# Kernel tuning notes

Hardware: AMD Instinct MI355X
Metric: run time of the kernel (lower is better)

Reference implementation:

```python
import jax, jax.numpy as jnp
import numpy as np

D_MODEL = 1024
NUM_HEADS = 16


def setup_inputs() -> dict:
    key = jax.random.key(0)
    ks = jax.random.split(key, 5)
    B, S, D = 2, 2048, D_MODEL
    scale = 1.0 / np.sqrt(D)
    return {
        "x": jax.random.normal(ks[0], (B, S, D), dtype=jnp.float32),
        "q_proj_weight": jax.random.normal(ks[1], (D, D), dtype=jnp.float32) * scale,
        "k_proj_weight": jax.random.normal(ks[2], (D, D), dtype=jnp.float32) * scale,
        "v_proj_weight": jax.random.normal(ks[3], (D, D), dtype=jnp.float32) * scale,
        "o_proj_weight": jax.random.normal(ks[4], (D, D), dtype=jnp.float32) * scale,
    }


def _attn(x, qw, kw, vw, ow, num_heads):
    B, S, D = x.shape
    d_k = D // num_heads
    q = x @ qw.T  # [B,S,D]
    k = x @ kw.T
    v = x @ vw.T
    # split heads: [B, H, S, d_k]
    q = q.reshape(B, S, num_heads, d_k).transpose(0, 2, 1, 3)
    k = k.reshape(B, S, num_heads, d_k).transpose(0, 2, 1, 3)
    v = v.reshape(B, S, num_heads, d_k).transpose(0, 2, 1, 3)
    scores = jnp.einsum('bhqd,bhkd->bhqk', q, k) / jnp.sqrt(jnp.asarray(d_k, x.dtype))
    causal = jnp.tril(jnp.ones((S, S), dtype=bool))  # [S,S]
    scores = jnp.where(causal[None, None], scores, jnp.asarray(-jnp.inf, x.dtype))
    attn = jax.nn.softmax(scores, axis=-1)
    out = jnp.einsum('bhqk,bhkd->bhqd', attn, v)  # [B,H,S,d_k]
    out = out.transpose(0, 2, 1, 3).reshape(B, S, D)
    return out @ ow.T


def reference(x, q_proj_weight, k_proj_weight, v_proj_weight, o_proj_weight):
    return _attn(x, q_proj_weight, k_proj_weight, v_proj_weight, o_proj_weight, NUM_HEADS)
```

## Files before the change

### kernel.cpp

```cpp
#include <hip/hip_runtime.h>

typedef __attribute__((ext_vector_type(8))) short short8;
typedef __attribute__((ext_vector_type(4))) float f32x4;

#define MFMA(a,b,c) __builtin_amdgcn_mfma_f32_16x16x32_bf16((a),(b),(c),0,0,0)

#define B_  2
#define S_  2048
#define D_  1024
#define H_  16
#define DK  64
#define KDIM 1024

typedef unsigned int u32;
typedef __attribute__((address_space(1))) const u32 gu32;
typedef __attribute__((address_space(3))) u32 lu32;

__device__ __forceinline__ void gll16(const unsigned short* g, unsigned short* l){
  __builtin_amdgcn_global_load_lds((gu32*)g, (lu32*)l, 16, 0, 0);
}

__device__ __forceinline__ unsigned short f2bf(float f){
  unsigned int u = __float_as_uint(f);
  u += 0x7fffu + ((u >> 16) & 1u);
  return (unsigned short)(u >> 16);
}

__device__ __forceinline__ u32 pkbf(float lo, float hi){
  u32 a = __float_as_uint(lo) + 0x8000u;
  u32 b = __float_as_uint(hi) + 0x8000u;
  return __builtin_amdgcn_perm(b, a, 0x07060302u);
}

__global__ void cvt_all(const float* __restrict__ x,  const float* __restrict__ qw,
                        const float* __restrict__ kw, const float* __restrict__ vw,
                        const float* __restrict__ ow,
                        unsigned short* __restrict__ xb,  unsigned short* __restrict__ wqb,
                        unsigned short* __restrict__ wkb, unsigned short* __restrict__ wvb,
                        unsigned short* __restrict__ wob,
                        int n4x, int n4w){
  int i = blockIdx.x * 256 + threadIdx.x;
  const float* src; unsigned short* dst; int n4;
  switch (blockIdx.y) {
    case 0:  src = x;  dst = xb;  n4 = n4x; break;
    case 1:  src = qw; dst = wqb; n4 = n4w; break;
    case 2:  src = kw; dst = wkb; n4 = n4w; break;
    case 3:  src = vw; dst = wvb; n4 = n4w; break;
    default: src = ow; dst = wob; n4 = n4w; break;
  }
  if (i >= n4) return;
  float4 f = reinterpret_cast<const float4*>(src)[i];
  ushort4 u;
  u.x = f2bf(f.x); u.y = f2bf(f.y); u.z = f2bf(f.z); u.w = f2bf(f.w);
  reinterpret_cast<ushort4*>(dst)[i] = u;
}

struct FragsQKV { short8 a0[4], a1[4], b0[3][2], b1[3][2]; };

__global__ __launch_bounds__(256, 2) void gemm_qkv(
    const unsigned short* __restrict__ X,
    const unsigned short* __restrict__ Wq,
    const unsigned short* __restrict__ Wk,
    const unsigned short* __restrict__ Wv,
    unsigned short* __restrict__ Qo,
    unsigned short* __restrict__ Ko,
    unsigned short* __restrict__ Vo)
{
  const int n0 = blockIdx.x * 64;
  const int m0 = blockIdx.y * 128;

  __shared__ unsigned short As[2][128 * 64];
  __shared__ unsigned short Bs[2][3][64 * 64];

  const int tid  = threadIdx.x;
  const int wid  = tid >> 6, lane = tid & 63;
  const int wm   = (wid >> 1) * 64, wn = (wid & 1) * 32;
  const int lr   = lane & 15, c = lane >> 4;
  const int sw   = lr & 7;
  const int pc0  = (c ^ sw) * 8;
  const int pc1  = ((c ^ 4) ^ sw) * 8;

  const int srow = lane >> 3;
  const int scol = ((lane & 7) ^ srow) * 8;
  const unsigned short* gA  = X  + (size_t)(m0 + wid * 32 + srow) * KDIM + scol;
  const unsigned short* gBq = Wq + (size_t)(n0 + wid * 16 + srow) * KDIM + scol;
  const unsigned short* gBk = Wk + (size_t)(n0 + wid * 16 + srow) * KDIM + scol;
  const unsigned short* gBv = Wv + (size_t)(n0 + wid * 16 + srow) * KDIM + scol;

  auto stage = [&](int buf, int k0) {
    unsigned short* la  = &As[buf][(wid * 32) * 64];
    unsigned short* lbq = &Bs[buf][0][(wid * 16) * 64];
    unsigned short* lbk = &Bs[buf][1][(wid * 16) * 64];
    unsigned short* lbv = &Bs[buf][2][(wid * 16) * 64];
#pragma unroll
    for (int i = 0; i < 4; i++) gll16(gA + (size_t)(i * 8) * KDIM + k0, la + i * 512);
#pragma unroll
    for (int i = 0; i < 2; i++) gll16(gBq + (size_t)(i * 8) * KDIM + k0, lbq + i * 512);
#pragma unroll
    for (int i = 0; i < 2; i++) gll16(gBk + (size_t)(i * 8) * KDIM + k0, lbk + i * 512);
#pragma unroll
    for (int i = 0; i < 2; i++) gll16(gBv + (size_t)(i * 8) * KDIM + k0, lbv + i * 512);
  };

  auto ldfr = [&](int buf, FragsQKV& f) {
    const unsigned short* AS = As[buf];
#pragma unroll
    for (int i = 0; i < 4; i++) {
      f.a0[i] = *(const short8*)&AS[(wm + i * 16 + lr) * 64 + pc0];
      f.a1[i] = *(const short8*)&AS[(wm + i * 16 + lr) * 64 + pc1];
    }
#pragma unroll
    for (int z = 0; z < 3; z++) {
      const unsigned short* BS = Bs[buf][z];
#pragma unroll
      for (int j = 0; j < 2; j++) {
        f.b0[z][j] = *(const short8*)&BS[(wn + j * 16 + lr) * 64 + pc0];
        f.b1[z][j] = *(const short8*)&BS[(wn + j * 16 + lr) * 64 + pc1];
      }
    }
  };

  f32x4 acc[3][4][2];
  const f32x4 z4 = {0.f, 0.f, 0.f, 0.f};
#pragma unroll
  for (int z = 0; z < 3; z++)
    for (int i = 0; i < 4; i++)
      for (int j = 0; j < 2; j++) acc[z][i][j] = z4;

  auto mfmas = [&](const FragsQKV& f) {
#pragma unroll
    for (int z = 0; z < 3; z++) {
      if (z == 2) {
#pragma unroll
        for (int i = 0; i < 4; i++)
#pragma unroll
          for (int j = 0; j < 2; j++) {
            acc[z][i][j] = MFMA(f.b0[z][j], f.a0[i], acc[z][i][j]);
            acc[z][i][j] = MFMA(f.b1[z][j], f.a1[i], acc[z][i][j]);
          }
      } else {
#pragma unroll
        for (int i = 0; i < 4; i++)
#pragma unroll
          for (int j = 0; j < 2; j++) {
            acc[z][i][j] = MFMA(f.a0[i], f.b0[z][j], acc[z][i][j]);
            acc[z][i][j] = MFMA(f.a1[i], f.b1[z][j], acc[z][i][j]);
          }
      }
    }
  };

  stage(0, 0);
  stage(1, 64);

  FragsQKV f;
  const int NT = KDIM / 64;
  for (int t = 0; t < NT - 2; ++t) {
    const int buf = t & 1;
    asm volatile("s_waitcnt vmcnt(10)" ::: "memory");
    __builtin_amdgcn_s_barrier();
    asm volatile("" ::: "memory");
    ldfr(buf, f);
    asm volatile("s_waitcnt lgkmcnt(0)" ::: "memory");
    __builtin_amdgcn_sched_barrier(0);
    __builtin_amdgcn_s_barrier();
    asm volatile("" ::: "memory");
    stage(buf, (t + 2) * 64);
    __builtin_amdgcn_sched_barrier(0);
    mfmas(f);
  }
  asm volatile("s_waitcnt vmcnt(10)" ::: "memory");
  __builtin_amdgcn_s_barrier();
  asm volatile("" ::: "memory");
  ldfr((NT - 2) & 1, f);
  mfmas(f);
  asm volatile("s_waitcnt vmcnt(0)" ::: "memory");
  __builtin_amdgcn_s_barrier();
  asm volatile("" ::: "memory");
  ldfr((NT - 1) & 1, f);
  mfmas(f);

  const int rbase = (lane >> 4) * 4;
  for (int i = 0; i < 4; i++)
    for (int j = 0; j < 2; j++)
      for (int r = 0; r < 4; r++) {
        int m = m0 + wm + i * 16 + rbase + r;
        int n = n0 + wn + j * 16 + lr;
        int bb = m >> 11, s = m & 2047, h = n >> 6, d = n & 63;
        float vq = acc[0][i][j][r] * 0.18033688f;
        Qo[(((bb * H_ + h) * S_) + s) * DK + d] = f2bf(vq);
        Ko[(((bb * H_ + h) * S_) + s) * DK + d] = f2bf(acc[1][i][j][r]);
      }
  for (int i = 0; i < 4; i++)
    for (int j = 0; j < 2; j++)
      for (int r = 0; r < 4; r++) {
        int dfull = n0 + wn + j * 16 + rbase + r;
        int sfull = m0 + wm + i * 16 + lr;
        int h = dfull >> 6, d = dfull & 63;
        int bb = sfull >> 11, s = sfull & 2047;
        Vo[(((bb * H_ + h) * DK) + d) * S_ + s] = f2bf(acc[2][i][j][r]);
      }
}

__global__ __launch_bounds__(512, 4) void attn(
    const unsigned short* __restrict__ Q,
    const unsigned short* __restrict__ K,
    const unsigned short* __restrict__ V,
    unsigned short* __restrict__ O)
{
  const int h = blockIdx.y, b = blockIdx.z;
  const int qt = b ? (15 - blockIdx.x) : blockIdx.x;

  const unsigned short* __restrict__ Qh = Q + (size_t)((b * H_ + h) * S_) * DK;
  const unsigned short* __restrict__ Kh = K + (size_t)((b * H_ + h) * S_) * DK;
  const unsigned short* __restrict__ Vh = V + (size_t)((b * H_ + h) * DK) * S_;

  __shared__ unsigned short Ks0[64 * 64];
  __shared__ unsigned short Ks1[64 * 64];
  __shared__ unsigned short Vs0[64 * 64];
  __shared__ unsigned short Vs1[64 * 64];
  __shared__ unsigned short Ps[8][16][72];

  const int tid = threadIdx.x, wid = tid >> 6, lane = tid & 63;
  const int lr = lane & 15;
  const int row4 = (lane >> 4) * 4;
  const int q0 = qt * 128;
  const int qcol = q0 + wid * 16 + lr;
  const int qwmin = q0 + wid * 16;
  const int qwmax = qwmin + 15;
  const int lk = (lane >> 4) * 8;

  const int pc0 = (((lane >> 4) + lr) & 7) * 8;
  const int pc1 = (((lane >> 4) + 4 + lr) & 7) * 8;

  const int sr8 = lane >> 3;
  const int sc8 = lane & 7;
  const int sg  = (sc8 - sr8) & 7;
  const int stRow = wid * 8 + sr8;
  const unsigned short* gK = Kh + (size_t)stRow * DK + sg * 8;
  const unsigned short* gV = Vh + (size_t)stRow * S_ + sg * 8;
  unsigned short* lK0 = &Ks0[wid * 8 * 64];
  unsigned short* lK1 = &Ks1[wid * 8 * 64];
  unsigned short* lV0 = &Vs0[wid * 8 * 64];
  unsigned short* lV1 = &Vs1[wid * 8 * 64];

  const short ONE = (short)0x3F80;
  const short8 ones = {ONE, ONE, ONE, ONE, ONE, ONE, ONE, ONE};

  short8 qf[2];
  qf[0] = *(const short8*)&Qh[(q0 + wid * 16 + lr) * DK + lk];
  qf[1] = *(const short8*)&Qh[(q0 + wid * 16 + lr) * DK + 32 + lk];

  const f32x4 z4 = {0.f, 0.f, 0.f, 0.f};
  f32x4 o[4];
  for (int i = 0; i < 4; i++) o[i] = z4;
  f32x4 rs = z4;

  auto tile = [&](int k0, const unsigned short* KS, const unsigned short* VS){
    if (k0 > qwmax) return;
    f32x4 sc[4];
    __builtin_amdgcn_s_setprio(1);
    for (int nt = 0; nt < 4; nt++) {
      short8 kb0 = *(const short8*)&KS[(nt * 16 + lr) * 64 + pc0];
      short8 kb1 = *(const short8*)&KS[(nt * 16 + lr) * 64 + pc1];
      f32x4 s = MFMA(kb0, qf[0], z4);
      sc[nt] = MFMA(kb1, qf[1], s);
    }
    __builtin_amdgcn_s_setprio(0);
    if (k0 + 63 > qwmin) {
      for (int nt = 0; nt < 4; nt++) {
        int kg = k0 + nt * 16 + row4;
        for (int r = 0; r < 4; r++)
          if (kg + r > qcol) sc[nt][r] = -INFINITY;
      }
    }
    for (int nt = 0; nt < 4; nt++) {
      float p0 = __builtin_amdgcn_exp2f(sc[nt][0]);
      float p1 = __builtin_amdgcn_exp2f(sc[nt][1]);
      float p2 = __builtin_amdgcn_exp2f(sc[nt][2]);
      float p3 = __builtin_amdgcn_exp2f(sc[nt][3]);
      uint2 pk;
      pk.x = pkbf(p0, p1);
      pk.y = pkbf(p2, p3);
      *(uint2*)&Ps[wid][lr][nt * 16 + row4] = pk;
    }
    short8 pf0 = *(const short8*)&Ps[wid][lr][lk];
    short8 pf1 = *(const short8*)&Ps[wid][lr][32 + lk];
    __builtin_amdgcn_s_setprio(1);
    rs = MFMA(ones, pf0, rs);
    rs = MFMA(ones, pf1, rs);
    for (int dt = 0; dt < 4; dt++) {
      short8 vb0 = *(const short8*)&VS[(dt * 16 + lr) * 64 + pc0];
      short8 vb1 = *(const short8*)&VS[(dt * 16 + lr) * 64 + pc1];
      o[dt] = MFMA(vb0, pf0, o[dt]);
      o[dt] = MFMA(vb1, pf1, o[dt]);
    }
    __builtin_amdgcn_s_setprio(0);
  };

  const int kt_end = 2 * qt + 2;

  gll16(gK, lK0);
  gll16(gV, lV0);

  for (int kt = 0; kt < kt_end; kt += 2) {
    const int k0 = kt * 64;
    __syncthreads();
    {
      gll16(gK + (size_t)(k0 + 64) * DK, lK1);
      gll16(gV + (k0 + 64),              lV1);
    }
    tile(k0, Ks0, Vs0);
    __syncthreads();
    if (kt + 2 < kt_end) {
      gll16(gK + (size_t)(k0 + 128) * DK, lK0);
      gll16(gV + (k0 + 128),              lV0);
    }
    tile(k0 + 64, Ks1, Vs1);
  }

  const float inv = 1.0f / rs[0];

  const int srow = q0 + wid * 16 + lr;
  for (int dt = 0; dt < 4; dt++) {
    uint2 pk;
    pk.x = pkbf(o[dt][0] * inv, o[dt][1] * inv);
    pk.y = pkbf(o[dt][2] * inv, o[dt][3] * inv);
    *(uint2*)&O[(size_t)(b * S_ + srow) * D_ + h * DK + dt * 16 + row4] = pk;
  }
}

struct Frags { short8 a0[4], a1[4], b0[2], b1[2]; };

__global__ __launch_bounds__(256) void gemm_oproj(
    const unsigned short* __restrict__ A,
    const unsigned short* __restrict__ W,
    float* __restrict__ out)
{
  const int n0 = blockIdx.x * 64;
  const int m0 = blockIdx.y * 128;

  __shared__ unsigned short As[2][128 * 64];
  __shared__ unsigned short Bs[2][64 * 64];

  const int tid  = threadIdx.x;
  const int wid  = tid >> 6, lane = tid & 63;
  const int wm   = (wid >> 1) * 64, wn = (wid & 1) * 32;
  const int lr   = lane & 15, c = lane >> 4;
  const int sw   = lr & 7;
  const int pc0  = (c ^ sw) * 8;
  const int pc1  = ((c ^ 4) ^ sw) * 8;

  const int srow = lane >> 3;
  const int scol = ((lane & 7) ^ srow) * 8;
  const unsigned short* gA = A + (size_t)(m0 + wid * 32 + srow) * KDIM + scol;
  const unsigned short* gB = W + (size_t)(n0 + wid * 16 + srow) * KDIM + scol;

  auto stage = [&](int buf, int k0) {
    unsigned short* la = &As[buf][(wid * 32) * 64];
    unsigned short* lb = &Bs[buf][(wid * 16) * 64];
#pragma unroll
    for (int i = 0; i < 4; i++) gll16(gA + (size_t)(i * 8) * KDIM + k0, la + i * 512);
#pragma unroll
    for (int i = 0; i < 2; i++) gll16(gB + (size_t)(i * 8) * KDIM + k0, lb + i * 512);
  };

  auto ldfr = [&](int buf, Frags& f) {
    const unsigned short* AS = As[buf];
    const unsigned short* BS = Bs[buf];
#pragma unroll
    for (int i = 0; i < 4; i++) {
      f.a0[i] = *(const short8*)&AS[(wm + i * 16 + lr) * 64 + pc0];
      f.a1[i] = *(const short8*)&AS[(wm + i * 16 + lr) * 64 + pc1];
    }
#pragma unroll
    for (int j = 0; j < 2; j++) {
      f.b0[j] = *(const short8*)&BS[(wn + j * 16 + lr) * 64 + pc0];
      f.b1[j] = *(const short8*)&BS[(wn + j * 16 + lr) * 64 + pc1];
    }
  };

  f32x4 acc[4][2];
  const f32x4 z4 = {0.f, 0.f, 0.f, 0.f};
  for (int i = 0; i < 4; i++)
    for (int j = 0; j < 2; j++) acc[i][j] = z4;

  auto mfmas = [&](const Frags& f) {
#pragma unroll
    for (int i = 0; i < 4; i++)
#pragma unroll
      for (int j = 0; j < 2; j++) {
        acc[i][j] = MFMA(f.a0[i], f.b0[j], acc[i][j]);
        acc[i][j] = MFMA(f.a1[i], f.b1[j], acc[i][j]);
      }
  };

  stage(0, 0);
  stage(1, 64);

  Frags f;
  const int NT = KDIM / 64;
  for (int t = 0; t < NT - 2; ++t) {
    const int buf = t & 1;
    asm volatile("s_waitcnt vmcnt(6)" ::: "memory");
    __builtin_amdgcn_s_barrier();
    asm volatile("" ::: "memory");
    ldfr(buf, f);
    asm volatile("s_waitcnt lgkmcnt(0)" ::: "memory");
    __builtin_amdgcn_sched_barrier(0);
    __builtin_amdgcn_s_barrier();
    asm volatile("" ::: "memory");
    stage(buf, (t + 2) * 64);
    __builtin_amdgcn_sched_barrier(0);
    mfmas(f);
  }
  asm volatile("s_waitcnt vmcnt(6)" ::: "memory");
  __builtin_amdgcn_s_barrier();
  asm volatile("" ::: "memory");
  ldfr((NT - 2) & 1, f);
  mfmas(f);
  asm volatile("s_waitcnt vmcnt(0)" ::: "memory");
  __builtin_amdgcn_s_barrier();
  asm volatile("" ::: "memory");
  ldfr((NT - 1) & 1, f);
  mfmas(f);

  const int rbase = (lane >> 4) * 4;
  for (int i = 0; i < 4; i++)
    for (int j = 0; j < 2; j++)
      for (int r = 0; r < 4; r++) {
        int m = m0 + wm + i * 16 + rbase + r;
        int n = n0 + wn + j * 16 + lr;
        out[(size_t)m * D_ + n] = acc[i][j][r];
      }
}

extern "C" void kernel_launch(void* const* d_in, const int* in_sizes, int n_in,
                              void* d_out, int out_size, void* d_ws, size_t ws_size,
                              hipStream_t stream) {
  const float* x  = (const float*)d_in[0];
  const float* qw = (const float*)d_in[1];
  const float* kw = (const float*)d_in[2];
  const float* vw = (const float*)d_in[3];
  const float* ow = (const float*)d_in[4];
  float* out = (float*)d_out;

  char* ws = (char*)d_ws;
  size_t off = 0;
  auto alloc = [&](size_t bytes) -> void* {
    void* p = ws + off;
    off += (bytes + 255) & ~(size_t)255;
    return p;
  };
  const size_t XN = (size_t)B_ * S_ * D_;
  const size_t WN = (size_t)D_ * D_;
  unsigned short* xb  = (unsigned short*)alloc(XN * 2);
  unsigned short* wqb = (unsigned short*)alloc(WN * 2);
  unsigned short* wkb = (unsigned short*)alloc(WN * 2);
  unsigned short* wvb = (unsigned short*)alloc(WN * 2);
  unsigned short* wob = (unsigned short*)alloc(WN * 2);
  unsigned short* Qb  = (unsigned short*)alloc(XN * 2);
  unsigned short* Kb  = (unsigned short*)alloc(XN * 2);
  unsigned short* Vb  = (unsigned short*)alloc(XN * 2);
  unsigned short* Ob  = (unsigned short*)alloc(XN * 2);

  cvt_all<<<dim3((XN / 4 + 255) / 256, 5), dim3(256), 0, stream>>>(
      x, qw, kw, vw, ow, xb, wqb, wkb, wvb, wob, (int)(XN / 4), (int)(WN / 4));

  gemm_qkv<<<dim3(D_ / 64, (B_ * S_) / 128), dim3(256), 0, stream>>>(
      xb, wqb, wkb, wvb, Qb, Kb, Vb);

  attn<<<dim3(S_ / 128, H_, B_), dim3(512), 0, stream>>>(Qb, Kb, Vb, Ob);

  gemm_oproj<<<dim3(D_ / 64, (B_ * S_) / 128), dim3(256), 0, stream>>>(Ob, wob, out);
}
```

Before: 152.6 us.

## Process 32 query rows per wave in attention, halving block size to 256 threads

The attention kernel now runs 4 waves per block instead of 8, each wave handling two 16-row query groups that share every K and V fragment read from LDS. Each thread issues twice as many async global-to-LDS loads to fill the same 64x64 K/V tiles. This halves LDS fragment traffic per MFMA and doubles MFMA work per wave. In exchange it raises register pressure (doubled accumulators and scores), lowers the launch-bound occupancy hint, and coarsens the causal early-exit to 32-row granularity.

```diff
diff --git a/kernel.cpp b/kernel.cpp
--- a/kernel.cpp
+++ b/kernel.cpp
@@ -202,7 +202,7 @@
       }
 }
 
-__global__ __launch_bounds__(512, 4) void attn(
+__global__ __launch_bounds__(256, 2) void attn(
     const unsigned short* __restrict__ Q,
     const unsigned short* __restrict__ K,
     const unsigned short* __restrict__ V,
@@ -219,15 +219,16 @@
   __shared__ unsigned short Ks1[64 * 64];
   __shared__ unsigned short Vs0[64 * 64];
   __shared__ unsigned short Vs1[64 * 64];
-  __shared__ unsigned short Ps[8][16][72];
+  __shared__ unsigned short Ps[4][32][72];
 
   const int tid = threadIdx.x, wid = tid >> 6, lane = tid & 63;
   const int lr = lane & 15;
   const int row4 = (lane >> 4) * 4;
   const int q0 = qt * 128;
-  const int qcol = q0 + wid * 16 + lr;
-  const int qwmin = q0 + wid * 16;
-  const int qwmax = qwmin + 15;
+  const int qw0 = q0 + wid * 32;
+  const int qcol0 = qw0 + lr;
+  const int qcol1 = qw0 + 16 + lr;
+  const int qwmax = qw0 + 31;
   const int lk = (lane >> 4) * 8;
 
   const int pc0 = (((lane >> 4) + lr) & 7) * 8;
@@ -236,97 +237,123 @@
   const int sr8 = lane >> 3;
   const int sc8 = lane & 7;
   const int sg  = (sc8 - sr8) & 7;
-  const int stRow = wid * 8 + sr8;
+  const int stRow = wid * 16 + sr8;
   const unsigned short* gK = Kh + (size_t)stRow * DK + sg * 8;
   const unsigned short* gV = Vh + (size_t)stRow * S_ + sg * 8;
-  unsigned short* lK0 = &Ks0[wid * 8 * 64];
-  unsigned short* lK1 = &Ks1[wid * 8 * 64];
-  unsigned short* lV0 = &Vs0[wid * 8 * 64];
-  unsigned short* lV1 = &Vs1[wid * 8 * 64];
+  unsigned short* lK0 = &Ks0[wid * 16 * 64];
+  unsigned short* lK1 = &Ks1[wid * 16 * 64];
+  unsigned short* lV0 = &Vs0[wid * 16 * 64];
+  unsigned short* lV1 = &Vs1[wid * 16 * 64];
 
   const short ONE = (short)0x3F80;
   const short8 ones = {ONE, ONE, ONE, ONE, ONE, ONE, ONE, ONE};
 
-  short8 qf[2];
-  qf[0] = *(const short8*)&Qh[(q0 + wid * 16 + lr) * DK + lk];
-  qf[1] = *(const short8*)&Qh[(q0 + wid * 16 + lr) * DK + 32 + lk];
+  short8 qf[2][2];
+  qf[0][0] = *(const short8*)&Qh[(size_t)qcol0 * DK + lk];
+  qf[0][1] = *(const short8*)&Qh[(size_t)qcol0 * DK + 32 + lk];
+  qf[1][0] = *(const short8*)&Qh[(size_t)qcol1 * DK + lk];
+  qf[1][1] = *(const short8*)&Qh[(size_t)qcol1 * DK + 32 + lk];
 
   const f32x4 z4 = {0.f, 0.f, 0.f, 0.f};
-  f32x4 o[4];
-  for (int i = 0; i < 4; i++) o[i] = z4;
-  f32x4 rs = z4;
+  f32x4 o[2][4];
+  for (int g = 0; g < 2; g++)
+    for (int i = 0; i < 4; i++) o[g][i] = z4;
+  f32x4 rs[2] = {z4, z4};
 
   auto tile = [&](int k0, const unsigned short* KS, const unsigned short* VS){
     if (k0 > qwmax) return;
-    f32x4 sc[4];
+    f32x4 sc[2][4];
     __builtin_amdgcn_s_setprio(1);
+#pragma unroll
     for (int nt = 0; nt < 4; nt++) {
       short8 kb0 = *(const short8*)&KS[(nt * 16 + lr) * 64 + pc0];
       short8 kb1 = *(const short8*)&KS[(nt * 16 + lr) * 64 + pc1];
-      f32x4 s = MFMA(kb0, qf[0], z4);
-      sc[nt] = MFMA(kb1, qf[1], s);
+      sc[0][nt] = MFMA(kb1, qf[0][1], MFMA(kb0, qf[0][0], z4));
+      sc[1][nt] = MFMA(kb1, qf[1][1], MFMA(kb0, qf[1][0], z4));
     }
     __builtin_amdgcn_s_setprio(0);
-    if (k0 + 63 > qwmin) {
+    if (k0 + 63 > qw0) {
+#pragma unroll
       for (int nt = 0; nt < 4; nt++) {
         int kg = k0 + nt * 16 + row4;
-        for (int r = 0; r < 4; r++)
-          if (kg + r > qcol) sc[nt][r] = -INFINITY;
-      }
-    }
-    for (int nt = 0; nt < 4; nt++) {
-      float p0 = __builtin_amdgcn_exp2f(sc[nt][0]);
-      float p1 = __builtin_amdgcn_exp2f(sc[nt][1]);
-      float p2 = __builtin_amdgcn_exp2f(sc[nt][2]);
-      float p3 = __builtin_amdgcn_exp2f(sc[nt][3]);
-      uint2 pk;
-      pk.x = pkbf(p0, p1);
-      pk.y = pkbf(p2, p3);
-      *(uint2*)&Ps[wid][lr][nt * 16 + row4] = pk;
-    }
-    short8 pf0 = *(const short8*)&Ps[wid][lr][lk];
-    short8 pf1 = *(const short8*)&Ps[wid][lr][32 + lk];
+#pragma unroll
+        for (int r = 0; r < 4; r++) {
+          if (kg + r > qcol0) sc[0][nt][r] = -INFINITY;
+          if (kg + r > qcol1) sc[1][nt][r] = -INFINITY;
+        }
+      }
+    }
+#pragma unroll
+    for (int g = 0; g < 2; g++)
+#pragma unroll
+      for (int nt = 0; nt < 4; nt++) {
+        float p0 = __builtin_amdgcn_exp2f(sc[g][nt][0]);
+        float p1 = __builtin_amdgcn_exp2f(sc[g][nt][1]);
+        float p2 = __builtin_amdgcn_exp2f(sc[g][nt][2]);
+        float p3 = __builtin_amdgcn_exp2f(sc[g][nt][3]);
+        uint2 pk;
+        pk.x = pkbf(p0, p1);
+        pk.y = pkbf(p2, p3);
+        *(uint2*)&Ps[wid][g * 16 + lr][nt * 16 + row4] = pk;
+      }
+    short8 pf[2][2];
+    pf[0][0] = *(const short8*)&Ps[wid][lr][lk];
+    pf[0][1] = *(const short8*)&Ps[wid][lr][32 + lk];
+    pf[1][0] = *(const short8*)&Ps[wid][16 + lr][lk];
+    pf[1][1] = *(const short8*)&Ps[wid][16 + lr][32 + lk];
     __builtin_amdgcn_s_setprio(1);
-    rs = MFMA(ones, pf0, rs);
-    rs = MFMA(ones, pf1, rs);
+    rs[0] = MFMA(ones, pf[0][0], rs[0]);
+    rs[0] = MFMA(ones, pf[0][1], rs[0]);
+    rs[1] = MFMA(ones, pf[1][0], rs[1]);
+    rs[1] = MFMA(ones, pf[1][1], rs[1]);
+#pragma unroll
     for (int dt = 0; dt < 4; dt++) {
       short8 vb0 = *(const short8*)&VS[(dt * 16 + lr) * 64 + pc0];
       short8 vb1 = *(const short8*)&VS[(dt * 16 + lr) * 64 + pc1];
-      o[dt] = MFMA(vb0, pf0, o[dt]);
-      o[dt] = MFMA(vb1, pf1, o[dt]);
+      o[0][dt] = MFMA(vb0, pf[0][0], o[0][dt]);
+      o[0][dt] = MFMA(vb1, pf[0][1], o[0][dt]);
+      o[1][dt] = MFMA(vb0, pf[1][0], o[1][dt]);
+      o[1][dt] = MFMA(vb1, pf[1][1], o[1][dt]);
     }
     __builtin_amdgcn_s_setprio(0);
   };
 
   const int kt_end = 2 * qt + 2;
 
-  gll16(gK, lK0);
-  gll16(gV, lV0);
+  gll16(gK,            lK0);
+  gll16(gK + 8 * DK,   lK0 + 512);
+  gll16(gV,            lV0);
+  gll16(gV + 8 * S_,   lV0 + 512);
 
   for (int kt = 0; kt < kt_end; kt += 2) {
     const int k0 = kt * 64;
     __syncthreads();
     {
-      gll16(gK + (size_t)(k0 + 64) * DK, lK1);
-      gll16(gV + (k0 + 64),              lV1);
+      gll16(gK + (size_t)(k0 + 64) * DK,          lK1);
+      gll16(gK + (size_t)(k0 + 64 + 8) * DK,      lK1 + 512);
+      gll16(gV + (k0 + 64),                       lV1);
+      gll16(gV + (k0 + 64) + 8 * S_,              lV1 + 512);
     }
     tile(k0, Ks0, Vs0);
     __syncthreads();
     if (kt + 2 < kt_end) {
-      gll16(gK + (size_t)(k0 + 128) * DK, lK0);
-      gll16(gV + (k0 + 128),              lV0);
+      gll16(gK + (size_t)(k0 + 128) * DK,         lK0);
+      gll16(gK + (size_t)(k0 + 128 + 8) * DK,     lK0 + 512);
+      gll16(gV + (k0 + 128),                      lV0);
+      gll16(gV + (k0 + 128) + 8 * S_,             lV0 + 512);
     }
     tile(k0 + 64, Ks1, Vs1);
   }
 
-  const float inv = 1.0f / rs[0];
-
-  const int srow = q0 + wid * 16 + lr;
-  for (int dt = 0; dt < 4; dt++) {
-    uint2 pk;
-    pk.x = pkbf(o[dt][0] * inv, o[dt][1] * inv);
-    pk.y = pkbf(o[dt][2] * inv, o[dt][3] * inv);
-    *(uint2*)&O[(size_t)(b * S_ + srow) * D_ + h * DK + dt * 16 + row4] = pk;
+  for (int g = 0; g < 2; g++) {
+    const float inv = 1.0f / rs[g][0];
+    const int srow = qw0 + g * 16 + lr;
+    for (int dt = 0; dt < 4; dt++) {
+      uint2 pk;
+      pk.x = pkbf(o[g][dt][0] * inv, o[g][dt][1] * inv);
+      pk.y = pkbf(o[g][dt][2] * inv, o[g][dt][3] * inv);
+      *(uint2*)&O[(size_t)(b * S_ + srow) * D_ + h * DK + dt * 16 + row4] = pk;
+    }
   }
 }
 
@@ -470,7 +497,7 @@
   gemm_qkv<<<dim3(D_ / 64, (B_ * S_) / 128), dim3(256), 0, stream>>>(
       xb, wqb, wkb, wvb, Qb, Kb, Vb);
 
-  attn<<<dim3(S_ / 128, H_, B_), dim3(512), 0, stream>>>(Qb, Kb, Vb, Ob);
+  attn<<<dim3(S_ / 128, H_, B_), dim3(256), 0, stream>>>(Qb, Kb, Vb, Ob);
 
   gemm_oproj<<<dim3(D_ / 64, (B_ * S_) / 128), dim3(256), 0, stream>>>(Ob, wob, out);
 }
```

New measurement: 159.0 us. 4.2% more time.

## Triple-buffer K/V tiles in attention with explicit vmcnt waits

Applied to the files above, without the earlier changes.

Replaces the double-buffered K/V staging in the causal attention kernel with a three-slot ring buffer that prefetches two tiles ahead. Each iteration now uses a partial s_waitcnt vmcnt plus a single barrier instead of two __syncthreads per pair of tiles, so global loads can stay in flight across tile computations. This costs extra LDS (one more 16 KB K/V pair), which may reduce occupancy at launch_bounds(512,4), and relies on hand-managed vmcnt counts being correct.

```diff
diff --git a/kernel.cpp b/kernel.cpp
--- a/kernel.cpp
+++ b/kernel.cpp
@@ -215,10 +215,8 @@
   const unsigned short* __restrict__ Kh = K + (size_t)((b * H_ + h) * S_) * DK;
   const unsigned short* __restrict__ Vh = V + (size_t)((b * H_ + h) * DK) * S_;
 
-  __shared__ unsigned short Ks0[64 * 64];
-  __shared__ unsigned short Ks1[64 * 64];
-  __shared__ unsigned short Vs0[64 * 64];
-  __shared__ unsigned short Vs1[64 * 64];
+  __shared__ unsigned short Ks[3][64 * 64];
+  __shared__ unsigned short Vs[3][64 * 64];
   __shared__ unsigned short Ps[8][16][72];
 
   const int tid = threadIdx.x, wid = tid >> 6, lane = tid & 63;
@@ -239,10 +237,8 @@
   const int stRow = wid * 8 + sr8;
   const unsigned short* gK = Kh + (size_t)stRow * DK + sg * 8;
   const unsigned short* gV = Vh + (size_t)stRow * S_ + sg * 8;
-  unsigned short* lK0 = &Ks0[wid * 8 * 64];
-  unsigned short* lK1 = &Ks1[wid * 8 * 64];
-  unsigned short* lV0 = &Vs0[wid * 8 * 64];
-  unsigned short* lV1 = &Vs1[wid * 8 * 64];
+  unsigned short* kd[3] = {&Ks[0][wid * 8 * 64], &Ks[1][wid * 8 * 64], &Ks[2][wid * 8 * 64]};
+  unsigned short* vd[3] = {&Vs[0][wid * 8 * 64], &Vs[1][wid * 8 * 64], &Vs[2][wid * 8 * 64]};
 
   const short ONE = (short)0x3F80;
   const short8 ones = {ONE, ONE, ONE, ONE, ONE, ONE, ONE, ONE};
@@ -298,25 +294,24 @@
     __builtin_amdgcn_s_setprio(0);
   };
 
-  const int kt_end = 2 * qt + 2;
-
-  gll16(gK, lK0);
-  gll16(gV, lV0);
-
-  for (int kt = 0; kt < kt_end; kt += 2) {
-    const int k0 = kt * 64;
-    __syncthreads();
-    {
-      gll16(gK + (size_t)(k0 + 64) * DK, lK1);
-      gll16(gV + (k0 + 64),              lV1);
-    }
-    tile(k0, Ks0, Vs0);
-    __syncthreads();
-    if (kt + 2 < kt_end) {
-      gll16(gK + (size_t)(k0 + 128) * DK, lK0);
-      gll16(gV + (k0 + 128),              lV0);
-    }
-    tile(k0 + 64, Ks1, Vs1);
+  const int T = 2 * qt + 2;
+
+  gll16(gK,                     kd[0]);
+  gll16(gV,                     vd[0]);
+  gll16(gK + (size_t)64 * DK,   kd[1]);
+  gll16(gV + 64,                vd[1]);
+
+  for (int t = 0; t < T; ++t) {
+    if (t < T - 1) asm volatile("s_waitcnt vmcnt(2)" ::: "memory");
+    else           asm volatile("s_waitcnt vmcnt(0)" ::: "memory");
+    __builtin_amdgcn_s_barrier();
+    asm volatile("" ::: "memory");
+    if (t + 2 < T) {
+      const int cbuf = (t + 2) % 3;
+      gll16(gK + (size_t)((t + 2) * 64) * DK, kd[cbuf]);
+      gll16(gV + (t + 2) * 64,                vd[cbuf]);
+    }
+    tile(t * 64, &Ks[t % 3][0], &Vs[t % 3][0]);
   }
 
   const float inv = 1.0f / rs[0];
```

Measured after the change: 161.4 us. 5.8% more time.

## Remap K rows so softmax probabilities stay in registers, dropping LDS P round-trip

Applied to the files above, without the earlier changes.

Permutes which K rows each lane's score-MFMA output covers so the P fragment produced by the QK^T MFMA already matches the B-operand layout of the PV MFMA. This removes the per-tile shared-memory store and reload of P (the Ps buffer) and the LDS traffic that went with it. To avoid bank conflicts under the new access pattern, the K tile is stored in LDS with a different swizzle, and the causal mask indices are updated to match. The risk is a subtle correctness error if the row permutation or swizzle does not line up.

```diff
diff --git a/kernel.cpp b/kernel.cpp
--- a/kernel.cpp
+++ b/kernel.cpp
@@ -2,6 +2,7 @@
 
 typedef __attribute__((ext_vector_type(8))) short short8;
 typedef __attribute__((ext_vector_type(4))) float f32x4;
+typedef __attribute__((ext_vector_type(4))) unsigned int u32x4;
 
 #define MFMA(a,b,c) __builtin_amdgcn_mfma_f32_16x16x32_bf16((a),(b),(c),0,0,0)
 
@@ -219,26 +220,30 @@
   __shared__ unsigned short Ks1[64 * 64];
   __shared__ unsigned short Vs0[64 * 64];
   __shared__ unsigned short Vs1[64 * 64];
-  __shared__ unsigned short Ps[8][16][72];
 
   const int tid = threadIdx.x, wid = tid >> 6, lane = tid & 63;
-  const int lr = lane & 15;
-  const int row4 = (lane >> 4) * 4;
+  const int lr = lane & 15, c = lane >> 4;
+  const int row4 = c * 4;
   const int q0 = qt * 128;
   const int qcol = q0 + wid * 16 + lr;
   const int qwmin = q0 + wid * 16;
   const int qwmax = qwmin + 15;
-  const int lk = (lane >> 4) * 8;
-
-  const int pc0 = (((lane >> 4) + lr) & 7) * 8;
-  const int pc1 = (((lane >> 4) + 4 + lr) & 7) * 8;
+  const int lk = c * 8;
+
+  const int pcV0 = ((c + lr) & 7) * 8;
+  const int pcV1 = ((c + 4 + lr) & 7) * 8;
+  const int s8 = (lr & 3) + 2 * (lr >> 2);
+  const int pcA = ((c + s8) & 7) * 8;
+  const int pcB = ((c + s8 + 4) & 7) * 8;
+  const int rowb = (8 * (lr >> 2) + (lr & 3)) * 64;
 
   const int sr8 = lane >> 3;
   const int sc8 = lane & 7;
-  const int sg  = (sc8 - sr8) & 7;
+  const int sgV = (sc8 - sr8) & 7;
+  const int sgK = (sc8 - sr8 - 2 * (wid & 3)) & 7;
   const int stRow = wid * 8 + sr8;
-  const unsigned short* gK = Kh + (size_t)stRow * DK + sg * 8;
-  const unsigned short* gV = Vh + (size_t)stRow * S_ + sg * 8;
+  const unsigned short* gK = Kh + (size_t)stRow * DK + sgK * 8;
+  const unsigned short* gV = Vh + (size_t)stRow * S_ + sgV * 8;
   unsigned short* lK0 = &Ks0[wid * 8 * 64];
   unsigned short* lK1 = &Ks1[wid * 8 * 64];
   unsigned short* lV0 = &Vs0[wid * 8 * 64];
@@ -260,38 +265,59 @@
     if (k0 > qwmax) return;
     f32x4 sc[4];
     __builtin_amdgcn_s_setprio(1);
-    for (int nt = 0; nt < 4; nt++) {
-      short8 kb0 = *(const short8*)&KS[(nt * 16 + lr) * 64 + pc0];
-      short8 kb1 = *(const short8*)&KS[(nt * 16 + lr) * 64 + pc1];
-      f32x4 s = MFMA(kb0, qf[0], z4);
-      sc[nt] = MFMA(kb1, qf[1], s);
+    {
+      short8 kb;
+      kb = *(const short8*)&KS[rowb + pcA];
+      f32x4 t0 = MFMA(kb, qf[0], z4);
+      kb = *(const short8*)&KS[rowb + pcB];
+      sc[0] = MFMA(kb, qf[1], t0);
+      kb = *(const short8*)&KS[rowb + 256 + pcB];
+      f32x4 t1 = MFMA(kb, qf[0], z4);
+      kb = *(const short8*)&KS[rowb + 256 + pcA];
+      sc[1] = MFMA(kb, qf[1], t1);
+      kb = *(const short8*)&KS[rowb + 2048 + pcA];
+      f32x4 t2 = MFMA(kb, qf[0], z4);
+      kb = *(const short8*)&KS[rowb + 2048 + pcB];
+      sc[2] = MFMA(kb, qf[1], t2);
+      kb = *(const short8*)&KS[rowb + 2304 + pcB];
+      f32x4 t3 = MFMA(kb, qf[0], z4);
+      kb = *(const short8*)&KS[rowb + 2304 + pcA];
+      sc[3] = MFMA(kb, qf[1], t3);
     }
     __builtin_amdgcn_s_setprio(0);
     if (k0 + 63 > qwmin) {
-      for (int nt = 0; nt < 4; nt++) {
-        int kg = k0 + nt * 16 + row4;
+#pragma unroll
+      for (int m = 0; m < 4; m++) {
+        int kg = k0 + 8 * c + 4 * (m & 1) + 32 * (m >> 1);
+#pragma unroll
         for (int r = 0; r < 4; r++)
-          if (kg + r > qcol) sc[nt][r] = -INFINITY;
-      }
-    }
-    for (int nt = 0; nt < 4; nt++) {
-      float p0 = __builtin_amdgcn_exp2f(sc[nt][0]);
-      float p1 = __builtin_amdgcn_exp2f(sc[nt][1]);
-      float p2 = __builtin_amdgcn_exp2f(sc[nt][2]);
-      float p3 = __builtin_amdgcn_exp2f(sc[nt][3]);
-      uint2 pk;
-      pk.x = pkbf(p0, p1);
-      pk.y = pkbf(p2, p3);
-      *(uint2*)&Ps[wid][lr][nt * 16 + row4] = pk;
-    }
-    short8 pf0 = *(const short8*)&Ps[wid][lr][lk];
-    short8 pf1 = *(const short8*)&Ps[wid][lr][32 + lk];
+          if (kg + r > qcol) sc[m][r] = -INFINITY;
+      }
+    }
+    u32 w[4][2];
+#pragma unroll
+    for (int m = 0; m < 4; m++) {
+      float e0 = __builtin_amdgcn_exp2f(sc[m][0]);
+      float e1 = __builtin_amdgcn_exp2f(sc[m][1]);
+      float e2 = __builtin_amdgcn_exp2f(sc[m][2]);
+      float e3 = __builtin_amdgcn_exp2f(sc[m][3]);
+      w[m][0] = pkbf(e0, e1);
+      w[m][1] = pkbf(e2, e3);
+    }
+    short8 pf0, pf1;
+    {
+      u32x4 a0 = {w[0][0], w[0][1], w[1][0], w[1][1]};
+      u32x4 a1 = {w[2][0], w[2][1], w[3][0], w[3][1]};
+      pf0 = *(short8*)&a0;
+      pf1 = *(short8*)&a1;
+    }
     __builtin_amdgcn_s_setprio(1);
     rs = MFMA(ones, pf0, rs);
     rs = MFMA(ones, pf1, rs);
+#pragma unroll
     for (int dt = 0; dt < 4; dt++) {
-      short8 vb0 = *(const short8*)&VS[(dt * 16 + lr) * 64 + pc0];
-      short8 vb1 = *(const short8*)&VS[(dt * 16 + lr) * 64 + pc1];
+      short8 vb0 = *(const short8*)&VS[(dt * 16 + lr) * 64 + pcV0];
+      short8 vb1 = *(const short8*)&VS[(dt * 16 + lr) * 64 + pcV1];
       o[dt] = MFMA(vb0, pf0, o[dt]);
       o[dt] = MFMA(vb1, pf1, o[dt]);
     }
```

Measured after the change: 154.2 us. No clear change (+1.1%).
